# Kernel tuning notes

Hardware: AMD Instinct MI355X
Metric: run time of the kernel (lower is better)

Reference implementation:

```python
import jax, jax.numpy as jnp
import numpy as np

DT = 0.05
DELAY = int(1.0 / DT)  # 20 steps of synaptic delay
NUM_ASCS = 2
R_MEM = 0.1     # membrane resistance
SIGMA_V = 1.0   # sigmoid smoothing of spiking nonlinearity
V_RESET = 0.0

B, T, IN, HID, OUT = 64, 200, 512, 1024, 512


def setup_inputs() -> dict:
    key = jax.random.key(0)
    ks = jax.random.split(key, 10)
    return {
        "x": jax.random.normal(ks[0], (B, T, IN), dtype=jnp.float32),
        "W_in": jax.random.normal(ks[1], (IN, HID), dtype=jnp.float32) / np.sqrt(IN),
        "W_lat": jax.random.normal(ks[2], (HID, HID), dtype=jnp.float32) / np.sqrt(HID),
        "thresh": jax.random.normal(ks[3], (1, HID), dtype=jnp.float32) * 0.1,
        "trans_k_m": jax.random.normal(ks[4], (1, HID), dtype=jnp.float32) * 0.1,
        "trans_asc_k": jax.random.normal(ks[5], (NUM_ASCS, 1, HID), dtype=jnp.float32) * 0.1,
        "asc_amp": jax.random.normal(ks[6], (NUM_ASCS, 1, HID), dtype=jnp.float32) * 0.1,
        "trans_asc_r": jax.random.normal(ks[7], (NUM_ASCS, 1, HID), dtype=jnp.float32) * 0.1,
        "W_out": jax.random.normal(ks[8], (OUT, HID), dtype=jnp.float32) / np.sqrt(HID),
        "b_out": jax.random.normal(ks[9], (OUT,), dtype=jnp.float32) * 0.01,
    }


def _glifr_rnn(x, W_in, W_lat, thresh, trans_k_m, trans_asc_k, asc_amp, trans_asc_r, W_out, b_out):
    Bx, Tx, _ = x.shape
    H = W_lat.shape[0]
    # rate transforms keep dt*k in (0,1); r in (-1,1)
    k_m = jax.nn.sigmoid(trans_k_m) / DT          # [1,H]
    k_asc = jax.nn.sigmoid(trans_asc_k) / DT      # [A,1,H]
    asc_r = 1.0 - 2.0 * jax.nn.sigmoid(trans_asc_r)
    # precompute input projection for all timesteps: [T,B,H]
    x_proj = jnp.swapaxes(jnp.einsum("bti,ih->bth", x, W_in), 0, 1)

    def step(carry, xp):
        firing, voltage, asc, buf = carry
        firing_delayed = buf[0]                       # firing DELAY steps ago
        syn = xp + firing_delayed @ W_lat             # synaptic current [B,H]
        asc_new = (asc_amp + asc_r * asc) * firing * (DT * k_asc) + (1.0 - DT * k_asc) * asc
        volt_new = (R_MEM * DT * k_m) * (syn + asc_new.sum(0)) \
                   + (1.0 - DT * k_m) * voltage + DT * k_m * V_RESET
        firing_new = jax.nn.sigmoid((volt_new - thresh) / SIGMA_V)
        buf_new = jnp.concatenate([buf[1:], firing_new[None]], axis=0)
        out = firing_new @ W_out.T + b_out            # per-step linear readout
        return (firing_new, volt_new, asc_new, buf_new), out

    z = jnp.zeros((Bx, H), dtype=x.dtype)
    carry0 = (z, z, jnp.zeros((NUM_ASCS, Bx, H), x.dtype), jnp.zeros((DELAY, Bx, H), x.dtype))
    _, outs = jax.lax.scan(step, carry0, x_proj)      # outs: [T,B,OUT]
    return jnp.swapaxes(outs, 0, 1)                   # [B,T,OUT]


def reference(x, W_in, W_lat, thresh, trans_k_m, trans_asc_k, asc_amp, trans_asc_r, W_out, b_out):
    return _glifr_rnn(x, W_in, W_lat, thresh, trans_k_m, trans_asc_k, asc_amp, trans_asc_r, W_out, b_out)
```

## Files before the change

kernel.cpp:

```cpp
#include <hip/hip_runtime.h>


typedef float f32x4 __attribute__((ext_vector_type(4)));
typedef __bf16 bf16x8 __attribute__((ext_vector_type(8)));
typedef unsigned short ushortx8 __attribute__((ext_vector_type(8)));
typedef unsigned short ushortx4 __attribute__((ext_vector_type(4)));

__device__ __forceinline__ unsigned short f2b(float f) {
    unsigned int u = __float_as_uint(f);
    unsigned int r = u + 0x7FFFu + ((u >> 16) & 1u);
    return (unsigned short)(r >> 16);
}
__device__ __forceinline__ float sigmoidf(float x) {
    return 1.0f / (1.0f + __expf(-x));
}

__device__ __forceinline__ void gl_lds16(const unsigned short* g, unsigned short* l) {
    __builtin_amdgcn_global_load_lds(
        (const __attribute__((address_space(1))) void*)g,
        (__attribute__((address_space(3))) void*)l, 16, 0, 0);
}

__global__ __launch_bounds__(256) void prep_all(
    const float* __restrict__ W_in, const float* __restrict__ W_lat,
    const float* __restrict__ W_out, const float* __restrict__ x,
    unsigned short* __restrict__ WinT, unsigned short* __restrict__ WlatT,
    unsigned short* __restrict__ WoutB, unsigned short* __restrict__ xb)
{
    __shared__ unsigned short t[64][65];
    const int blk = blockIdx.x, tid = threadIdx.x;

    if (blk < 128) {
        int bx = (blk & 15) * 64, by = (blk >> 4) * 64;
        int tx = tid & 63, ty = tid >> 6;
        for (int r = ty; r < 64; r += 4)
            t[r][tx] = f2b(W_in[(size_t)(by + r) * 1024 + bx + tx]);
        __syncthreads();
        for (int r = ty; r < 64; r += 4)
            WinT[(size_t)(bx + r) * 512 + by + tx] = t[tx][r];
    } else if (blk < 384) {
        int b2 = blk - 128;
        int bx = (b2 & 15) * 64, by = (b2 >> 4) * 64;
        int tx = tid & 63, ty = tid >> 6;
        for (int r = ty; r < 64; r += 4)
            t[r][tx] = f2b(W_lat[(size_t)(by + r) * 1024 + bx + tx]);
        __syncthreads();
        for (int r = ty; r < 64; r += 4)
            WlatT[(size_t)(bx + r) * 1024 + by + tx] = t[tx][r];
    } else if (blk < 896) {
        int i = ((blk - 384) * 256 + tid) * 4;
        f32x4 v = *(const f32x4*)(W_out + i);
        ushortx4 o;
        o[0] = f2b(v[0]); o[1] = f2b(v[1]); o[2] = f2b(v[2]); o[3] = f2b(v[3]);
        *(ushortx4*)(WoutB + i) = o;
    } else {
        size_t i8 = (size_t)((blk - 896) * 256 + tid) * 8;
        int m = (int)(i8 >> 9), k = (int)(i8 & 511);
        int b = m & 63, tt = m >> 6;
        const float* src = x + ((size_t)b * 200 + tt) * 512 + k;
        f32x4 v0 = *(const f32x4*)src;
        f32x4 v1 = *(const f32x4*)(src + 4);
        ushortx8 o;
        o[0] = f2b(v0[0]); o[1] = f2b(v0[1]); o[2] = f2b(v0[2]); o[3] = f2b(v0[3]);
        o[4] = f2b(v1[0]); o[5] = f2b(v1[1]); o[6] = f2b(v1[2]); o[7] = f2b(v1[3]);
        *(ushortx8*)(xb + i8) = o;
    }
}

template<int BM, int BN, int MODE>
__global__ __launch_bounds__(256) void gemm_nt(
    const unsigned short* __restrict__ A,
    const unsigned short* __restrict__ Bt,
    float* __restrict__ outf,
    const float* __restrict__ bias,
    int M, int N, int K, int t_base)
{
    constexpr int WM = BM / 2, WN = BN / 2;
    constexpr int TM = WM / 16, TN = WN / 16;

    __shared__ unsigned short Asm[BM * 64];
    __shared__ unsigned short Bsm[BN * 64];

    const int tid  = threadIdx.x;
    const int wave = tid >> 6, lane = tid & 63;
    const int m16  = lane & 15, quad = lane >> 4;
    const int bm0  = blockIdx.y * BM, bn0 = blockIdx.x * BN;
    const int wr   = (wave >> 1) * WM, wc = (wave & 1) * WN;
    const int sr   = lane >> 3;
    const int sc   = lane & 7;

    f32x4 acc[TM][TN];
#pragma unroll
    for (int i = 0; i < TM; i++)
#pragma unroll
        for (int j = 0; j < TN; j++)
            acc[i][j] = (f32x4){0.f, 0.f, 0.f, 0.f};

    for (int k0 = 0; k0 < K; k0 += 64) {
#pragma unroll
        for (int g = wave; g < BM / 8; g += 4) {
            int r = g * 8 + sr;
            int c = sc ^ (r & 7);
            gl_lds16(A + (size_t)(bm0 + r) * K + k0 + c * 8, Asm + g * 512);
        }
#pragma unroll
        for (int g = wave; g < BN / 8; g += 4) {
            int r = g * 8 + sr;
            int c = sc ^ (r & 7);
            gl_lds16(Bt + (size_t)(bn0 + r) * K + k0 + c * 8, Bsm + g * 512);
        }
        __syncthreads();

        ushortx8 af[2][TM], bfr[2][TN];
#pragma unroll
        for (int kh = 0; kh < 2; kh++) {
#pragma unroll
            for (int i = 0; i < TM; i++) {
                int ra = wr + i * 16 + m16;
                af[kh][i] = *(const ushortx8*)(
                    Asm + ra * 64 + (((kh * 4 + quad) ^ (ra & 7)) * 8));
            }
#pragma unroll
            for (int j = 0; j < TN; j++) {
                int rb = wc + j * 16 + m16;
                bfr[kh][j] = *(const ushortx8*)(
                    Bsm + rb * 64 + (((kh * 4 + quad) ^ (rb & 7)) * 8));
            }
        }
#pragma unroll
        for (int i = 0; i < TM; i++)
#pragma unroll
            for (int j = 0; j < TN; j++) {
                acc[i][j] = __builtin_amdgcn_mfma_f32_16x16x32_bf16(
                    __builtin_bit_cast(bf16x8, af[0][i]),
                    __builtin_bit_cast(bf16x8, bfr[0][j]),
                    acc[i][j], 0, 0, 0);
                acc[i][j] = __builtin_amdgcn_mfma_f32_16x16x32_bf16(
                    __builtin_bit_cast(bf16x8, af[1][i]),
                    __builtin_bit_cast(bf16x8, bfr[1][j]),
                    acc[i][j], 0, 0, 0);
            }
        __syncthreads();
    }

#pragma unroll
    for (int i = 0; i < TM; i++)
#pragma unroll
        for (int j = 0; j < TN; j++) {
            int col = bn0 + wc + j * 16 + m16;
            float bv = (MODE == 2) ? bias[col] : 0.f;
#pragma unroll
            for (int v = 0; v < 4; v++) {
                int row = bm0 + wr + i * 16 + quad * 4 + v;
                if (MODE == 2) {
                    size_t o = (size_t)((row & 63) * 200 + t_base + (row >> 6)) * N + col;
                    outf[o] = acc[i][j][v] + bv;
                } else {
                    outf[(size_t)row * N + col] = acc[i][j][v];
                }
            }
        }
}

__global__ __launch_bounds__(256) void fused_chunk(
    const unsigned short* __restrict__ Fprev,
    const unsigned short* __restrict__ Wlat,
    const float* __restrict__ xproj,
    float* __restrict__ state,
    unsigned short* __restrict__ Fc,
    const float* __restrict__ thresh,
    const float* __restrict__ t_km,
    const float* __restrict__ t_ak,
    const float* __restrict__ amp,
    const float* __restrict__ t_ar)
{
    const int BH = 64 * 1024;
    __shared__ __align__(16) char lds[147456];
    unsigned short* Asm = (unsigned short*)lds;
    unsigned short* Bsm = (unsigned short*)(lds + 81920);
    float* synT = (float*)lds;

    const int tid  = threadIdx.x;
    const int wave = tid >> 6, lane = tid & 63;
    const int m16  = lane & 15, quad = lane >> 4;
    const int b0   = blockIdx.y * 4, h0 = blockIdx.x * 64;
    const int wrow = (wave >> 1) * 48;
    const int wc   = (wave & 1) * 32;

    f32x4 acc[3][2];
#pragma unroll
    for (int i = 0; i < 3; i++) {
        if (i < 2 || wave < 2) {
#pragma unroll
            for (int j = 0; j < 2; j++)
#pragma unroll
                for (int v = 0; v < 4; v++) {
                    int row = wrow + i * 16 + quad * 4 + v;
                    int col = h0 + wc + j * 16 + m16;
                    acc[i][j][v] = xproj[(size_t)(((row >> 2) << 6) + b0 + (row & 3)) * 1024 + col];
                }
        }
    }

    for (int k0 = 0; k0 < 1024; k0 += 512) {
        for (int g = wave; g < 80; g += 4) {
            int c = lane ^ (g & 63);
            int m = ((g >> 2) << 6) + b0 + (g & 3);
            gl_lds16(Fprev + (size_t)m * 1024 + k0 + c * 8, Asm + g * 512);
        }
        for (int g = wave; g < 64; g += 4) {
            int c = lane ^ (g & 63);
            gl_lds16(Wlat + (size_t)(h0 + g) * 1024 + k0 + c * 8, Bsm + g * 512);
        }
        __syncthreads();

#pragma unroll
        for (int qt = 0; qt < 4; qt++) {
            ushortx8 af[4][3], bfr[4][2];
#pragma unroll
            for (int kh = 0; kh < 4; kh++) {
                int s = qt * 16 + kh * 4 + quad;
#pragma unroll
                for (int i = 0; i < 3; i++) {
                    if (i < 2 || wave < 2) {
                        int ra = wrow + i * 16 + m16;
                        af[kh][i] = *(const ushortx8*)(
                            Asm + ra * 512 + ((s ^ (ra & 63)) * 8));
                    }
                }
#pragma unroll
                for (int j = 0; j < 2; j++) {
                    int rb = wc + j * 16 + m16;
                    bfr[kh][j] = *(const ushortx8*)(
                        Bsm + rb * 512 + ((s ^ (rb & 63)) * 8));
                }
            }
#pragma unroll
            for (int i = 0; i < 3; i++) {
                if (i < 2 || wave < 2) {
#pragma unroll
                    for (int j = 0; j < 2; j++) {
#pragma unroll
                        for (int kh = 0; kh < 4; kh++) {
                            acc[i][j] = __builtin_amdgcn_mfma_f32_16x16x32_bf16(
                                __builtin_bit_cast(bf16x8, af[kh][i]),
                                __builtin_bit_cast(bf16x8, bfr[kh][j]), acc[i][j], 0, 0, 0);
                        }
                    }
                }
            }
        }
        __syncthreads();
    }

#pragma unroll
    for (int i = 0; i < 3; i++) {
        if (i < 2 || wave < 2) {
#pragma unroll
            for (int j = 0; j < 2; j++)
#pragma unroll
                for (int v = 0; v < 4; v++) {
                    int row = wrow + i * 16 + quad * 4 + v;
                    synT[row * 66 + wc + j * 16 + m16] = acc[i][j][v];
                }
        }
    }
    __syncthreads();

    const int h    = h0 + lane;
    const int gidx = (b0 + wave) * 1024 + h;
    float th  = thresh[h];
    float sm  = sigmoidf(t_km[h]);
    float rm  = 0.1f * sm;
    float om  = 1.0f - sm;
    float sa0 = sigmoidf(t_ak[h]);
    float sa1 = sigmoidf(t_ak[1024 + h]);
    float am0 = amp[h];
    float am1 = amp[1024 + h];
    float r0  = 1.0f - 2.0f * sigmoidf(t_ar[h]);
    float r1  = 1.0f - 2.0f * sigmoidf(t_ar[1024 + h]);

    float volt = state[gidx];
    float a0   = state[BH + gidx];
    float a1   = state[2 * BH + gidx];
    float fir  = state[3 * BH + gidx];

#pragma unroll
    for (int s = 0; s < 20; s++) {
        float sv  = synT[(s * 4 + wave) * 66 + lane];
        float na0 = (am0 + r0 * a0) * fir * sa0 + (1.f - sa0) * a0;
        float na1 = (am1 + r1 * a1) * fir * sa1 + (1.f - sa1) * a1;
        volt = rm * (sv + na0 + na1) + om * volt;
        fir  = sigmoidf(volt - th);
        Fc[(size_t)s * BH + gidx] = f2b(fir);
        a0 = na0; a1 = na1;
    }
    state[gidx]          = volt;
    state[BH + gidx]     = a0;
    state[2 * BH + gidx] = a1;
    state[3 * BH + gidx] = fir;
}

__global__ __launch_bounds__(256) void chunk_step(
    const float* __restrict__ syn,
    float* __restrict__ state,
    unsigned short* __restrict__ F,
    const float* __restrict__ thresh,
    const float* __restrict__ t_km,
    const float* __restrict__ t_ak,
    const float* __restrict__ amp,
    const float* __restrict__ t_ar)
{
    const int BH = 64 * 1024;
    int idx = blockIdx.x * 256 + threadIdx.x;
    int h = idx & 1023;

    float th  = thresh[h];
    float sm  = sigmoidf(t_km[h]);
    float rm  = 0.1f * sm;
    float om  = 1.0f - sm;
    float sa0 = sigmoidf(t_ak[h]);
    float sa1 = sigmoidf(t_ak[1024 + h]);
    float am0 = amp[h];
    float am1 = amp[1024 + h];
    float r0  = 1.0f - 2.0f * sigmoidf(t_ar[h]);
    float r1  = 1.0f - 2.0f * sigmoidf(t_ar[1024 + h]);

    float volt = 0.f, a0 = 0.f, a1 = 0.f, fir = 0.f;

#pragma unroll
    for (int s = 0; s < 20; s++) {
        float sv  = syn[(size_t)s * BH + idx];
        float na0 = (am0 + r0 * a0) * fir * sa0 + (1.f - sa0) * a0;
        float na1 = (am1 + r1 * a1) * fir * sa1 + (1.f - sa1) * a1;
        volt = rm * (sv + na0 + na1) + om * volt;
        fir  = sigmoidf(volt - th);
        F[(size_t)s * BH + idx] = f2b(fir);
        a0 = na0; a1 = na1;
    }
    state[idx]          = volt;
    state[BH + idx]     = a0;
    state[2 * BH + idx] = a1;
    state[3 * BH + idx] = fir;
}

extern "C" void kernel_launch(void* const* d_in, const int* in_sizes, int n_in,
                              void* d_out, int out_size, void* d_ws, size_t ws_size,
                              hipStream_t stream)
{
    const float* x      = (const float*)d_in[0];
    const float* W_in   = (const float*)d_in[1];
    const float* W_lat  = (const float*)d_in[2];
    const float* thresh = (const float*)d_in[3];
    const float* t_km   = (const float*)d_in[4];
    const float* t_ak   = (const float*)d_in[5];
    const float* amp    = (const float*)d_in[6];
    const float* t_ar   = (const float*)d_in[7];
    const float* W_out  = (const float*)d_in[8];
    const float* b_out  = (const float*)d_in[9];
    float* out = (float*)d_out;

    char* ws = (char*)d_ws;
    float*          syn   = (float*)ws;
    float*          state = (float*)(ws + 52428800);
    unsigned short* F     = (unsigned short*)(ws + 53477376);
    unsigned short* xb    = F;
    unsigned short* WinT  = (unsigned short*)(ws + 79691776);
    unsigned short* WlatT = (unsigned short*)(ws + 80740352);
    unsigned short* WoutB = (unsigned short*)(ws + 82837504);

    prep_all<<<4096, 256, 0, stream>>>(W_in, W_lat, W_out, x,
                                       WinT, WlatT, WoutB, xb);

    gemm_nt<128, 128, 0><<<dim3(1024 / 128, 12800 / 128), 256, 0, stream>>>(
        xb, WinT, syn, nullptr, 12800, 1024, 512, 0);

    chunk_step<<<256, 256, 0, stream>>>(syn, state, F, thresh, t_km, t_ak, amp, t_ar);

    const size_t CHUNK = 20 * 64 * 1024;
    for (int c = 1; c < 10; c++) {
        fused_chunk<<<dim3(16, 16), 256, 0, stream>>>(
            F + (size_t)(c - 1) * CHUNK, WlatT,
            syn + (size_t)c * CHUNK, state, F + (size_t)c * CHUNK,
            thresh, t_km, t_ak, amp, t_ar);
    }

    gemm_nt<128, 128, 2><<<dim3(512 / 128, 12800 / 128), 256, 0, stream>>>(
        F, WoutB, out, b_out, 12800, 512, 1024, 0);
}
```

Baseline: 256.4 us.

## Double-buffer K-chunks of the lateral GEMM to overlap loads with MFMA

New measurement: 252.8 us. Within noise of the previous version (-1.4%).

```diff
diff --git a/kernel.cpp b/kernel.cpp
--- a/kernel.cpp
+++ b/kernel.cpp
@@ -176,13 +176,17 @@
 {
     const int BH = 64 * 1024;
     __shared__ __align__(16) char lds[147456];
-    unsigned short* Asm = (unsigned short*)lds;
-    unsigned short* Bsm = (unsigned short*)(lds + 81920);
+    unsigned short* A0 = (unsigned short*)lds;
+    unsigned short* A1 = (unsigned short*)(lds + 40960);
+    unsigned short* B0 = (unsigned short*)(lds + 81920);
+    unsigned short* B1 = (unsigned short*)(lds + 114688);
     float* synT = (float*)lds;
 
     const int tid  = threadIdx.x;
     const int wave = tid >> 6, lane = tid & 63;
     const int m16  = lane & 15, quad = lane >> 4;
+    const int sr2  = lane >> 5;
+    const int sc32 = lane & 31;
     const int b0   = blockIdx.y * 4, h0 = blockIdx.x * 64;
     const int wrow = (wave >> 1) * 48;
     const int wc   = (wave & 1) * 32;
@@ -202,37 +206,39 @@
         }
     }
 
-    for (int k0 = 0; k0 < 1024; k0 += 512) {
-        for (int g = wave; g < 80; g += 4) {
-            int c = lane ^ (g & 63);
-            int m = ((g >> 2) << 6) + b0 + (g & 3);
-            gl_lds16(Fprev + (size_t)m * 1024 + k0 + c * 8, Asm + g * 512);
-        }
-        for (int g = wave; g < 64; g += 4) {
-            int c = lane ^ (g & 63);
-            gl_lds16(Wlat + (size_t)(h0 + g) * 1024 + k0 + c * 8, Bsm + g * 512);
-        }
-        __syncthreads();
-
-#pragma unroll
-        for (int qt = 0; qt < 4; qt++) {
+    auto STAGE = [&](unsigned short* Ad, unsigned short* Bd, int k0) {
+        for (int g = wave; g < 40; g += 4) {
+            int r = g * 2 + sr2;
+            int c = sc32 ^ (r & 31);
+            int m = ((r >> 2) << 6) + b0 + (r & 3);
+            gl_lds16(Fprev + (size_t)m * 1024 + k0 + c * 8, Ad + g * 512);
+        }
+        for (int g = wave; g < 32; g += 4) {
+            int r = g * 2 + sr2;
+            int c = sc32 ^ (r & 31);
+            gl_lds16(Wlat + (size_t)(h0 + r) * 1024 + k0 + c * 8, Bd + g * 512);
+        }
+    };
+    auto COMPUTE = [&](const unsigned short* As, const unsigned short* Bs) {
+#pragma unroll
+        for (int half = 0; half < 2; half++) {
             ushortx8 af[4][3], bfr[4][2];
 #pragma unroll
             for (int kh = 0; kh < 4; kh++) {
-                int s = qt * 16 + kh * 4 + quad;
+                int s = half * 16 + kh * 4 + quad;
 #pragma unroll
                 for (int i = 0; i < 3; i++) {
                     if (i < 2 || wave < 2) {
                         int ra = wrow + i * 16 + m16;
                         af[kh][i] = *(const ushortx8*)(
-                            Asm + ra * 512 + ((s ^ (ra & 63)) * 8));
+                            As + ra * 256 + ((s ^ (ra & 31)) * 8));
                     }
                 }
 #pragma unroll
                 for (int j = 0; j < 2; j++) {
                     int rb = wc + j * 16 + m16;
                     bfr[kh][j] = *(const ushortx8*)(
-                        Bsm + rb * 512 + ((s ^ (rb & 63)) * 8));
+                        Bs + rb * 256 + ((s ^ (rb & 31)) * 8));
                 }
             }
 #pragma unroll
@@ -250,8 +256,14 @@
                 }
             }
         }
-        __syncthreads();
-    }
+    };
+
+    STAGE(A0, B0, 0);
+    __syncthreads();
+    STAGE(A1, B1, 256);  COMPUTE(A0, B0);  __syncthreads();
+    STAGE(A0, B0, 512);  COMPUTE(A1, B1);  __syncthreads();
+    STAGE(A1, B1, 768);  COMPUTE(A0, B0);  __syncthreads();
+                         COMPUTE(A1, B1);  __syncthreads();
 
 #pragma unroll
     for (int i = 0; i < 3; i++) {
```
